# Optimization experiments

Measured on AMD Instinct MI355X. Metric: run time of the kernel, lower is better.

Reference implementation:

```python
import jax, jax.numpy as jnp
import numpy as np

N = 32768      # total nodes
E = 524288     # edges (avg degree 16)
HID = 256      # hidden_dim
H = 8          # heads
C = HID // H   # head dim = 32
G = 64         # graphs in batch
NPG = N // G   # nodes per graph = 512
EDIM = 2       # edge feature dim
NEG_SLOPE = 0.2  # PyG GATv2 default


def setup_inputs():
    key = jax.random.key(0)
    ks = jax.random.split(key, 12)
    s = 0.05
    return dict(
        x=jax.random.normal(ks[0], (N, HID), jnp.float32),
        edge_attr=jax.random.normal(ks[1], (E, EDIM), jnp.float32),
        # GATv2Conv params
        W_l=jax.random.normal(ks[2], (HID, HID), jnp.float32) * s,
        b_l=jnp.zeros((HID,), jnp.float32),
        W_r=jax.random.normal(ks[3], (HID, HID), jnp.float32) * s,
        b_r=jnp.zeros((HID,), jnp.float32),
        W_e=jax.random.normal(ks[4], (EDIM, HID), jnp.float32) * s,
        att=jax.random.normal(ks[5], (H, C), jnp.float32) * s,
        bias_gat=jnp.zeros((HID,), jnp.float32),
        # MultiheadAttention params (torch packed qkv layout)
        in_proj_w=jax.random.normal(ks[6], (3 * HID, HID), jnp.float32) * s,
        in_proj_b=jnp.zeros((3 * HID,), jnp.float32),
        out_proj_w=jax.random.normal(ks[7], (HID, HID), jnp.float32) * s,
        out_proj_b=jnp.zeros((HID,), jnp.float32),
        alpha_param=jnp.array(0.5, jnp.float32),
        # FFN
        W1=jax.random.normal(ks[8], (HID, 4 * HID), jnp.float32) * s,
        b1=jnp.zeros((4 * HID,), jnp.float32),
        W2=jax.random.normal(ks[9], (4 * HID, HID), jnp.float32) * s,
        b2=jnp.zeros((HID,), jnp.float32),
        # LayerNorms
        g1=jnp.ones((HID,), jnp.float32), be1=jnp.zeros((HID,), jnp.float32),
        g2=jnp.ones((HID,), jnp.float32), be2=jnp.zeros((HID,), jnp.float32),
        g3=jnp.ones((HID,), jnp.float32), be3=jnp.zeros((HID,), jnp.float32),
        edge_index=jax.random.randint(ks[10], (2, E), 0, N, jnp.int32),
        batch=jnp.repeat(jnp.arange(G, dtype=jnp.int32), NPG),
    )


def _ln(x, g, b, eps=1e-5):
    m = jnp.mean(x, -1, keepdims=True)
    v = jnp.mean((x - m) ** 2, -1, keepdims=True)
    return (x - m) * jax.lax.rsqrt(v + eps) * g + b


def _gatv2(x, edge_index, edge_attr, W_l, b_l, W_r, b_r, W_e, att, bias_gat):
    src, dst = edge_index[0], edge_index[1]
    # PyG add_self_loops with fill_value='mean': self-loop edge_attr at node i
    # is the mean of edge_attr over edges incoming to i (0 if none).
    deg = jax.ops.segment_sum(jnp.ones((E,), x.dtype), dst, num_segments=N)
    ea_mean = jax.ops.segment_sum(edge_attr, dst, num_segments=N) / jnp.maximum(deg, 1.0)[:, None]
    loop = jnp.arange(N, dtype=src.dtype)
    src2 = jnp.concatenate([src, loop])
    dst2 = jnp.concatenate([dst, loop])
    ea2 = jnp.concatenate([edge_attr, ea_mean], axis=0)  # [E+N, 2]
    xl = (x @ W_l + b_l).reshape(N, H, C)  # source transform (messages)
    xr = (x @ W_r + b_r).reshape(N, H, C)  # target transform
    ee = (ea2 @ W_e).reshape(-1, H, C)
    e = jax.nn.leaky_relu(xl[src2] + xr[dst2] + ee, NEG_SLOPE)  # [E+N, H, C]
    score = jnp.einsum('ehc,hc->eh', e, att)  # [E+N, H]
    # scatter softmax over incoming edges of each target node
    smax = jax.lax.stop_gradient(jax.ops.segment_max(score, dst2, num_segments=N))
    ex = jnp.exp(score - smax[dst2])
    ssum = jax.ops.segment_sum(ex, dst2, num_segments=N)
    alpha = ex / ssum[dst2]  # [E+N, H]
    out = jax.ops.segment_sum(alpha[:, :, None] * xl[src2], dst2, num_segments=N)
    return out.reshape(N, HID) + bias_gat


def _mha(xg, in_proj_w, in_proj_b, out_proj_w, out_proj_b):
    # xg: [G, NPG, HID]; torch nn.MultiheadAttention (batch_first, eval mode)
    qkv = xg @ in_proj_w.T + in_proj_b
    q, k, v = jnp.split(qkv, 3, axis=-1)
    q = q.reshape(G, NPG, H, C)
    k = k.reshape(G, NPG, H, C)
    v = v.reshape(G, NPG, H, C)
    scores = jnp.einsum('gqhd,gkhd->ghqk', q, k) / jnp.sqrt(jnp.float32(C))
    p = jax.nn.softmax(scores, axis=-1)
    o = jnp.einsum('ghqk,gkhd->gqhd', p, v).reshape(G, NPG, HID)
    return o @ out_proj_w.T + out_proj_b


def reference(x, edge_attr, W_l, b_l, W_r, b_r, W_e, att, bias_gat,
              in_proj_w, in_proj_b, out_proj_w, out_proj_b, alpha_param,
              W1, b1, W2, b2, g1, be1, g2, be2, g3, be3, edge_index, batch):
    local_out = _ln(
        _gatv2(x, edge_index, edge_attr, W_l, b_l, W_r, b_r, W_e, att, bias_gat),
        g1, be1)
    # batch is sorted with equal-sized graphs -> the per-graph ragged
    # attention loop equals one batched [G, NPG, NPG] attention
    xg = x.reshape(G, NPG, HID)
    global_out = _mha(xg, in_proj_w, in_proj_b, out_proj_w, out_proj_b).reshape(N, HID)
    global_out = _ln(global_out, g2, be2)
    a = jax.nn.sigmoid(alpha_param)
    combined = a * local_out + (1.0 - a) * global_out
    ffn = jax.nn.gelu(combined @ W1 + b1, approximate=False) @ W2 + b2
    return _ln(combined + ffn, g3, be3)
```

## Files before the change

### kernel.cpp

```cpp
#include <hip/hip_runtime.h>
#include <math.h>

#define N_NODES 32768
#define E_EDGES 524288
#define HIDDEN  256
#define NPG     512
#define NGRAPH  64
#define NHEAD   8
#define CDIM    32

typedef unsigned short bf16;
typedef __attribute__((ext_vector_type(8))) short short8;
typedef __attribute__((ext_vector_type(4))) float f4;

#define AS1 __attribute__((address_space(1)))
#define AS3 __attribute__((address_space(3)))

__device__ __forceinline__ void cp16(const bf16* g, bf16* l) {
    __builtin_amdgcn_global_load_lds((AS1 const unsigned int*)(const void*)g,
                                     (AS3 unsigned int*)(void*)l, 16, 0, 0);
}

__device__ inline float bf2f(unsigned short u) {
    union { unsigned int i; float f; } v; v.i = ((unsigned int)u) << 16; return v.f;
}
__device__ inline unsigned short f2bf(float f) {
    union { float f; unsigned int i; } v; v.f = f;
    unsigned int x = v.i;
    return (unsigned short)((x + 0x7FFFu + ((x >> 16) & 1u)) >> 16);
}
__device__ inline float4 load4(const float* p) { return *(const float4*)p; }
__device__ inline float4 load4(const bf16* p) {
    ushort4 u = *(const ushort4*)p;
    return make_float4(bf2f(u.x), bf2f(u.y), bf2f(u.z), bf2f(u.w));
}
__device__ inline void store4(float* p, float4 v) { *(float4*)p = v; }
__device__ inline void store4(bf16* p, float4 v) {
    ushort4 u; u.x = f2bf(v.x); u.y = f2bf(v.y); u.z = f2bf(v.z); u.w = f2bf(v.w);
    *(ushort4*)p = u;
}


__global__ void zero_kernel(float* deg, float* ea_sum, int* fill) {
    int i = blockIdx.x * blockDim.x + threadIdx.x;
    if (i < 2 * N_NODES) ea_sum[i] = 0.0f;
    if (i < N_NODES) { deg[i] = 0.0f; fill[i] = 0; }
}

__global__ void deg_kernel(const int* __restrict__ ei, const float* __restrict__ edge_attr,
                           float* deg, float* ea_sum) {
    int e = blockIdx.x * blockDim.x + threadIdx.x;
    if (e >= E_EDGES) return;
    int d = ei[E_EDGES + e];
    atomicAdd(&deg[d], 1.0f);
    atomicAdd(&ea_sum[2 * d + 0], edge_attr[2 * e + 0]);
    atomicAdd(&ea_sum[2 * d + 1], edge_attr[2 * e + 1]);
}

__global__ void eamean_kernel(const float* __restrict__ deg, float* ea_mean) {
    int i = blockIdx.x * blockDim.x + threadIdx.x;
    if (i >= N_NODES) return;
    float dm = fmaxf(deg[i], 1.0f);
    ea_mean[2 * i + 0] /= dm;
    ea_mean[2 * i + 1] /= dm;
}

__global__ __launch_bounds__(1024) void scan_kernel(const float* __restrict__ deg, int* row_ptr) {
    __shared__ int part[1024];
    int t = threadIdx.x;
    int base = t * 32;
    int loc[32];
    int s = 0;
    #pragma unroll
    for (int j = 0; j < 32; j++) {
        loc[j] = s;
        s += (int)deg[base + j] + 1;
    }
    int mysum = s;
    part[t] = s;
    __syncthreads();
    for (int off = 1; off < 1024; off <<= 1) {
        int v = 0;
        if (t >= off) v = part[t - off];
        __syncthreads();
        part[t] += v;
        __syncthreads();
    }
    int offset = part[t] - mysum;
    #pragma unroll
    for (int j = 0; j < 32; j++) row_ptr[base + j] = offset + loc[j];
    if (t == 1023) row_ptr[N_NODES] = part[1023];
}

__global__ void fill_kernel(const int* __restrict__ ei, const float* __restrict__ edge_attr,
                            const float* __restrict__ ea_mean,
                            const int* __restrict__ row_ptr, int* fill, int4* __restrict__ erec) {
    int tid = blockIdx.x * blockDim.x + threadIdx.x;
    if (tid >= E_EDGES + N_NODES) return;
    int d, src; float a0, a1;
    if (tid < E_EDGES) {
        d = ei[E_EDGES + tid];
        src = ei[tid];
        a0 = edge_attr[2 * tid + 0];
        a1 = edge_attr[2 * tid + 1];
    } else {
        d = tid - E_EDGES;
        src = d;
        a0 = ea_mean[2 * d + 0];
        a1 = ea_mean[2 * d + 1];
    }
    int pos = row_ptr[d] + atomicAdd(&fill[d], 1);
    int4 r;
    r.x = src;
    r.y = __float_as_int(a0);
    r.z = __float_as_int(a1);
    r.w = 0;
    erec[pos] = r;
}

__global__ void convall(const float* __restrict__ x,
                        const float* __restrict__ W_l, const float* __restrict__ W_r,
                        const float* __restrict__ W1, const float* __restrict__ W2,
                        const float* __restrict__ in_proj_w, const float* __restrict__ out_proj_w,
                        const float* __restrict__ b_l, const float* __restrict__ b_r,
                        bf16* xb, bf16* wlrb, bf16* w1b, bf16* w2b,
                        bf16* wipb, bf16* wopb, float* blr)
{
    int b = blockIdx.x, t = threadIdx.x;
    if (b < 8192) {
        int i = b * 256 + t;
        store4(&xb[i * 4], *(const float4*)&x[i * 4]);
    } else if (b < 8448) {
        int i = (b - 8192) * 256 + t; int k = i >> 8, n = i & 255;
        wlrb[n * 256 + k] = f2bf(W_l[i]);
    } else if (b < 8704) {
        int i = (b - 8448) * 256 + t; int k = i >> 8, n = i & 255;
        wlrb[(256 + n) * 256 + k] = f2bf(W_r[i]);
    } else if (b < 9728) {
        int i = (b - 8704) * 256 + t; int k = i >> 10, n = i & 1023;
        w1b[n * 256 + k] = f2bf(W1[i]);
    } else if (b < 10752) {
        int i = (b - 9728) * 256 + t; int k = i >> 8, n = i & 255;
        w2b[n * 1024 + k] = f2bf(W2[i]);
    } else if (b < 10944) {
        int i = (b - 10752) * 256 + t;
        store4(&wipb[i * 4], *(const float4*)&in_proj_w[i * 4]);
    } else if (b < 11008) {
        int i = (b - 10944) * 256 + t;
        store4(&wopb[i * 4], *(const float4*)&out_proj_w[i * 4]);
    } else {
        blr[t] = b_l[t]; blr[256 + t] = b_r[t];
    }
}

template <int EPI>
__global__ __launch_bounds__(256) void mfma_gemm(
    const bf16* __restrict__ A, const bf16* __restrict__ Wb,
    const float* __restrict__ bias, const bf16* __restrict__ res,
    bf16* __restrict__ C, int M, int N, int K)
{
    __shared__ bf16 lds[2 * 128 * 64];
    bf16* As = lds;
    bf16* Bs = lds + 128 * 64;
    int tid = threadIdx.x;
    int wave = tid >> 6, lane = tid & 63;
    int quad = lane >> 4, l16 = lane & 15;
    int n0 = blockIdx.x * 128, m0 = blockIdx.y * 128;
    int wm = (wave & 1) * 64, wn = (wave >> 1) * 64;

    f4 acc[4][4] = {};

    int srow = tid >> 3;
    int scol = (tid & 7) * 8;

    for (int k0 = 0; k0 < K; k0 += 64) {
        #pragma unroll
        for (int i = 0; i < 4; i++) {
            int row = i * 32 + srow;
            cp16(&A[(size_t)(m0 + row) * K + k0 + scol], &As[row * 64 + scol]);
            cp16(&Wb[(size_t)(n0 + row) * K + k0 + scol], &Bs[row * 64 + scol]);
        }
        __syncthreads();
        #pragma unroll
        for (int ks = 0; ks < 2; ks++) {
            short8 af[4], bfr[4];
            #pragma unroll
            for (int mt = 0; mt < 4; mt++)
                af[mt] = *(const short8*)&As[(wm + mt * 16 + l16) * 64 + ks * 32 + quad * 8];
            #pragma unroll
            for (int nt = 0; nt < 4; nt++)
                bfr[nt] = *(const short8*)&Bs[(wn + nt * 16 + l16) * 64 + ks * 32 + quad * 8];
            #pragma unroll
            for (int mt = 0; mt < 4; mt++)
                #pragma unroll
                for (int nt = 0; nt < 4; nt++)
                    acc[mt][nt] = __builtin_amdgcn_mfma_f32_16x16x32_bf16(
                        af[mt], bfr[nt], acc[mt][nt], 0, 0, 0);
        }
        __syncthreads();
    }

    float* epi = (float*)lds + wave * 16 * 68;
    int row = lane >> 2;
    int cb = (lane & 3) * 16;
    int gn = n0 + wn + cb;
    float bb[16];
    *(float4*)&bb[0]  = *(const float4*)&bias[gn + 0];
    *(float4*)&bb[4]  = *(const float4*)&bias[gn + 4];
    *(float4*)&bb[8]  = *(const float4*)&bias[gn + 8];
    *(float4*)&bb[12] = *(const float4*)&bias[gn + 12];

    for (int mt = 0; mt < 4; mt++) {
        #pragma unroll
        for (int nt = 0; nt < 4; nt++)
            #pragma unroll
            for (int r = 0; r < 4; r++)
                epi[(quad * 4 + r) * 68 + nt * 16 + l16] = acc[mt][nt][r];
        float vv[16];
        *(float4*)&vv[0]  = *(float4*)&epi[row * 68 + cb + 0];
        *(float4*)&vv[4]  = *(float4*)&epi[row * 68 + cb + 4];
        *(float4*)&vv[8]  = *(float4*)&epi[row * 68 + cb + 8];
        *(float4*)&vv[12] = *(float4*)&epi[row * 68 + cb + 12];
        int gm = m0 + wm + mt * 16 + row;
        #pragma unroll
        for (int j = 0; j < 16; j++) vv[j] += bb[j];
        if (EPI == 1) {
            #pragma unroll
            for (int j = 0; j < 16; j++)
                vv[j] = 0.5f * vv[j] * (1.0f + erff(vv[j] * 0.70710678118654752f));
        } else if (EPI == 2) {
            ushort rr[16];
            const bf16* rp = &res[(size_t)gm * N + gn];
            *(int4*)&rr[0] = *(const int4*)&rp[0];
            *(int4*)&rr[8] = *(const int4*)&rp[8];
            #pragma unroll
            for (int j = 0; j < 16; j++) vv[j] += bf2f(rr[j]);
        }
        ushort o16[16];
        #pragma unroll
        for (int j = 0; j < 16; j++) o16[j] = f2bf(vv[j]);
        bf16* cp;
        if (EPI == 3) {
            bf16* dst = (gn < 256) ? C : (bf16*)res;
            int goff = (gn < 256) ? gn : gn - 256;
            cp = &dst[(size_t)gm * 256 + goff];
        } else {
            cp = &C[(size_t)gm * N + gn];
        }
        *(int4*)&cp[0] = *(int4*)&o16[0];
        *(int4*)&cp[8] = *(int4*)&o16[8];
    }
}

__global__ __launch_bounds__(256) void attn_mfma(
    const bf16* __restrict__ qkv, bf16* __restrict__ attnout)
{
    __shared__ bf16 Ks[128 * 40];
    __shared__ bf16 Vt[32 * 136];
    __shared__ bf16 Pb[4 * 64 * 40];

    int b = blockIdx.x;
    int g = b >> 4, h = (b >> 1) & 7, hlf = b & 1;
    int tid = threadIdx.x;
    int wave = tid >> 6, lane = tid & 63;
    int quad = lane >> 4, l16 = lane & 15;
    int qbase = hlf * 256 + wave * 64;
    bf16* Pw = &Pb[wave * 64 * 40];
    const float SCALE = 0.17677669529663687f;

    short8 qf[4];
    #pragma unroll
    for (int mt = 0; mt < 4; mt++) {
        size_t node = (size_t)(g * NPG + qbase + mt * 16 + l16);
        qf[mt] = *(const short8*)&qkv[node * 768 + h * CDIM + quad * 8];
    }

    f4 oacc[4][2] = {};
    float lacc[4][4] = {};

    for (int c = 0; c < 4; c++) {
        int kk0 = c * 128;
        __syncthreads();
        #pragma unroll
        for (int i = 0; i < 2; i++) {
            int idx = i * 256 + tid;
            int key = idx >> 2, kc = (idx & 3) * 8;
            *(int4*)&Ks[key * 40 + kc] =
                *(const int4*)&qkv[(size_t)(g * NPG + kk0 + key) * 768 + 256 + h * CDIM + kc];
        }
        {
            int key = tid >> 1, dblk = (tid & 1) * 16;
            ushort tmp[16];
            const bf16* vp = &qkv[(size_t)(g * NPG + kk0 + key) * 768 + 512 + h * CDIM + dblk];
            *(int4*)&tmp[0] = *(const int4*)&vp[0];
            *(int4*)&tmp[8] = *(const int4*)&vp[8];
            #pragma unroll
            for (int j = 0; j < 16; j++) Vt[(dblk + j) * 136 + key] = tmp[j];
        }
        __syncthreads();

        for (int sub = 0; sub < 4; sub++) {
            int ks0 = sub * 32;
            short8 kf[2];
            #pragma unroll
            for (int nt = 0; nt < 2; nt++)
                kf[nt] = *(const short8*)&Ks[(ks0 + nt * 16 + l16) * 40 + quad * 8];
            #pragma unroll
            for (int mt = 0; mt < 4; mt++) {
                #pragma unroll
                for (int nt = 0; nt < 2; nt++) {
                    f4 z = {0.f, 0.f, 0.f, 0.f};
                    f4 s = __builtin_amdgcn_mfma_f32_16x16x32_bf16(qf[mt], kf[nt], z, 0, 0, 0);
                    #pragma unroll
                    for (int r = 0; r < 4; r++) {
                        float p = __expf(s[r] * SCALE);
                        lacc[mt][r] += p;
                        Pw[(mt * 16 + quad * 4 + r) * 40 + nt * 16 + l16] = f2bf(p);
                    }
                }
            }
            short8 vf[2];
            #pragma unroll
            for (int dt = 0; dt < 2; dt++)
                vf[dt] = *(const short8*)&Vt[(dt * 16 + l16) * 136 + ks0 + quad * 8];
            #pragma unroll
            for (int mt = 0; mt < 4; mt++) {
                short8 pf = *(const short8*)&Pw[(mt * 16 + l16) * 40 + quad * 8];
                #pragma unroll
                for (int dt = 0; dt < 2; dt++)
                    oacc[mt][dt] = __builtin_amdgcn_mfma_f32_16x16x32_bf16(
                        pf, vf[dt], oacc[mt][dt], 0, 0, 0);
            }
        }
    }

    #pragma unroll
    for (int mt = 0; mt < 4; mt++)
        #pragma unroll
        for (int r = 0; r < 4; r++) {
            float l = lacc[mt][r];
            l += __shfl_xor(l, 1);
            l += __shfl_xor(l, 2);
            l += __shfl_xor(l, 4);
            l += __shfl_xor(l, 8);
            lacc[mt][r] = l;
        }

    #pragma unroll
    for (int mt = 0; mt < 4; mt++) {
        #pragma unroll
        for (int dt = 0; dt < 2; dt++) {
            #pragma unroll
            for (int r = 0; r < 4; r++) {
                float v = oacc[mt][dt][r] / lacc[mt][r];
                size_t node = (size_t)(g * NPG + qbase + mt * 16 + quad * 4 + r);
                attnout[node * HIDDEN + h * CDIM + dt * 16 + l16] = f2bf(v);
            }
        }
    }
}

__device__ __forceinline__ void fetchrec(
    int i, int re, int node, const int4* __restrict__ erec,
    int& s, float& a0, float& a1)
{
    if (i < re) {
        int4 r = erec[i];
        s = r.x; a0 = __int_as_float(r.y); a1 = __int_as_float(r.z);
    } else {
        s = node; a0 = 0.f; a1 = 0.f;
    }
}

__global__ __launch_bounds__(256) void gat_kernel(
    const bf16* __restrict__ xl, const bf16* __restrict__ xr,
    const int* __restrict__ row_ptr, const int4* __restrict__ erec,
    const float* __restrict__ W_e, const float* __restrict__ att,
    const float* __restrict__ bias_gat,
    const float* __restrict__ g1, const float* __restrict__ be1,
    bf16* __restrict__ out)
{
    __shared__ float pacc[2][260];
    __shared__ float plsum[2][64];
    int wave = threadIdx.x >> 6;
    int lane = threadIdx.x & 63;
    int nloc = wave >> 1, half = wave & 1;
    int node = blockIdx.x * 2 + nloc;
    int cb = lane * 4;

    float4 xr4 = load4(&xr[(size_t)node * 256 + cb]);
    float4 we0 = *(const float4*)&W_e[cb];
    float4 we1 = *(const float4*)&W_e[HIDDEN + cb];
    float4 at4 = *(const float4*)&att[cb];

    int rs = row_ptr[node], re = row_ptr[node + 1];

    float lsum = 0.f;
    float acc0 = 0.f, acc1 = 0.f, acc2 = 0.f, acc3 = 0.f;

    int i0 = rs + half;
    int s0, s1; float a00, a01, a10, a11;
    fetchrec(i0,     re, node, erec, s0, a00, a01);
    fetchrec(i0 + 2, re, node, erec, s1, a10, a11);
    ushort4 xu0 = *(const ushort4*)&xl[(size_t)s0 * 256 + cb];

    for (int i = i0; i < re; i += 2) {
        int s2; float a20, a21;
        fetchrec(i + 4, re, node, erec, s2, a20, a21);
        ushort4 xu1 = *(const ushort4*)&xl[(size_t)s1 * 256 + cb];

        float4 xl4 = make_float4(bf2f(xu0.x), bf2f(xu0.y), bf2f(xu0.z), bf2f(xu0.w));
        float t, p = 0.f;
        t = xl4.x + xr4.x + a00 * we0.x + a01 * we1.x; t = (t > 0.f) ? t : 0.2f * t; p += t * at4.x;
        t = xl4.y + xr4.y + a00 * we0.y + a01 * we1.y; t = (t > 0.f) ? t : 0.2f * t; p += t * at4.y;
        t = xl4.z + xr4.z + a00 * we0.z + a01 * we1.z; t = (t > 0.f) ? t : 0.2f * t; p += t * at4.z;
        t = xl4.w + xr4.w + a00 * we0.w + a01 * we1.w; t = (t > 0.f) ? t : 0.2f * t; p += t * at4.w;
        p += __shfl_xor(p, 1);
        p += __shfl_xor(p, 2);
        p += __shfl_xor(p, 4);
        float w = __expf(p);
        lsum += w;
        acc0 += w * xl4.x; acc1 += w * xl4.y; acc2 += w * xl4.z; acc3 += w * xl4.w;

        s0 = s1; a00 = a10; a01 = a11; xu0 = xu1;
        s1 = s2; a10 = a20; a11 = a21;
    }

    if (half) {
        plsum[nloc][lane] = lsum;
        pacc[nloc][cb + 0] = acc0; pacc[nloc][cb + 1] = acc1;
        pacc[nloc][cb + 2] = acc2; pacc[nloc][cb + 3] = acc3;
    }
    __syncthreads();
    if (!half) {
        lsum += plsum[nloc][lane];
        acc0 += pacc[nloc][cb + 0]; acc1 += pacc[nloc][cb + 1];
        acc2 += pacc[nloc][cb + 2]; acc3 += pacc[nloc][cb + 3];

        float inv = 1.0f / lsum;
        float v0 = acc0 * inv + bias_gat[cb + 0];
        float v1 = acc1 * inv + bias_gat[cb + 1];
        float v2 = acc2 * inv + bias_gat[cb + 2];
        float v3 = acc3 * inv + bias_gat[cb + 3];

        float s = v0 + v1 + v2 + v3;
        #pragma unroll
        for (int m = 1; m < 64; m <<= 1) s += __shfl_xor(s, m);
        float mean = s * (1.0f / 256.0f);
        float d0 = v0 - mean, d1 = v1 - mean, d2 = v2 - mean, d3 = v3 - mean;
        float sq = d0 * d0 + d1 * d1 + d2 * d2 + d3 * d3;
        #pragma unroll
        for (int m = 1; m < 64; m <<= 1) sq += __shfl_xor(sq, m);
        float rstd = rsqrtf(sq * (1.0f / 256.0f) + 1e-5f);
        float4 o;
        o.x = d0 * rstd * g1[cb + 0] + be1[cb + 0];
        o.y = d1 * rstd * g1[cb + 1] + be1[cb + 1];
        o.z = d2 * rstd * g1[cb + 2] + be1[cb + 2];
        o.w = d3 * rstd * g1[cb + 3] + be1[cb + 3];
        store4(&out[(size_t)node * HIDDEN + cb], o);
    }
}

__global__ __launch_bounds__(256) void combine_kernel(
    const bf16* __restrict__ gout, const bf16* __restrict__ localout,
    const float* __restrict__ alpha_p,
    const float* __restrict__ g2, const float* __restrict__ be2,
    bf16* __restrict__ combined)
{
    int wave = threadIdx.x >> 6;
    int lane = threadIdx.x & 63;
    int node = blockIdx.x * 4 + wave;
    int cb = lane * 4;
    float4 gv = load4(&gout[(size_t)node * HIDDEN + cb]);
    float s = gv.x + gv.y + gv.z + gv.w;
    #pragma unroll
    for (int m = 1; m < 64; m <<= 1) s += __shfl_xor(s, m);
    float mean = s * (1.0f / 256.0f);
    float d0 = gv.x - mean, d1 = gv.y - mean, d2 = gv.z - mean, d3 = gv.w - mean;
    float sq = d0 * d0 + d1 * d1 + d2 * d2 + d3 * d3;
    #pragma unroll
    for (int m = 1; m < 64; m <<= 1) sq += __shfl_xor(sq, m);
    float rstd = rsqrtf(sq * (1.0f / 256.0f) + 1e-5f);
    float n0 = d0 * rstd * g2[cb + 0] + be2[cb + 0];
    float n1 = d1 * rstd * g2[cb + 1] + be2[cb + 1];
    float n2 = d2 * rstd * g2[cb + 2] + be2[cb + 2];
    float n3 = d3 * rstd * g2[cb + 3] + be2[cb + 3];
    float a = 1.0f / (1.0f + __expf(-alpha_p[0]));
    float4 lv = load4(&localout[(size_t)node * HIDDEN + cb]);
    float4 o;
    o.x = a * lv.x + (1.0f - a) * n0;
    o.y = a * lv.y + (1.0f - a) * n1;
    o.z = a * lv.z + (1.0f - a) * n2;
    o.w = a * lv.w + (1.0f - a) * n3;
    store4(&combined[(size_t)node * HIDDEN + cb], o);
}

__global__ __launch_bounds__(256) void finalln_kernel(
    const bf16* __restrict__ ffn,
    const float* __restrict__ g3, const float* __restrict__ be3,
    float* __restrict__ out)
{
    int wave = threadIdx.x >> 6;
    int lane = threadIdx.x & 63;
    int node = blockIdx.x * 4 + wave;
    int cb = lane * 4;
    float4 v = load4(&ffn[(size_t)node * HIDDEN + cb]);
    float s = v.x + v.y + v.z + v.w;
    #pragma unroll
    for (int m = 1; m < 64; m <<= 1) s += __shfl_xor(s, m);
    float mean = s * (1.0f / 256.0f);
    float d0 = v.x - mean, d1 = v.y - mean, d2 = v.z - mean, d3 = v.w - mean;
    float sq = d0 * d0 + d1 * d1 + d2 * d2 + d3 * d3;
    #pragma unroll
    for (int m = 1; m < 64; m <<= 1) sq += __shfl_xor(sq, m);
    float rstd = rsqrtf(sq * (1.0f / 256.0f) + 1e-5f);
    float4 o;
    o.x = d0 * rstd * g3[cb + 0] + be3[cb + 0];
    o.y = d1 * rstd * g3[cb + 1] + be3[cb + 1];
    o.z = d2 * rstd * g3[cb + 2] + be3[cb + 2];
    o.w = d3 * rstd * g3[cb + 3] + be3[cb + 3];
    *(float4*)&out[(size_t)node * HIDDEN + cb] = o;
}

extern "C" void kernel_launch(void* const* d_in, const int* in_sizes, int n_in,
                              void* d_out, int out_size, void* d_ws, size_t ws_size,
                              hipStream_t stream) {
    const float* x          = (const float*)d_in[0];
    const float* edge_attr  = (const float*)d_in[1];
    const float* W_l        = (const float*)d_in[2];
    const float* b_l        = (const float*)d_in[3];
    const float* W_r        = (const float*)d_in[4];
    const float* b_r        = (const float*)d_in[5];
    const float* W_e        = (const float*)d_in[6];
    const float* att        = (const float*)d_in[7];
    const float* bias_gat   = (const float*)d_in[8];
    const float* in_proj_w  = (const float*)d_in[9];
    const float* in_proj_b  = (const float*)d_in[10];
    const float* out_proj_w = (const float*)d_in[11];
    const float* out_proj_b = (const float*)d_in[12];
    const float* alpha_p    = (const float*)d_in[13];
    const float* W1         = (const float*)d_in[14];
    const float* b1         = (const float*)d_in[15];
    const float* W2         = (const float*)d_in[16];
    const float* b2         = (const float*)d_in[17];
    const float* g1  = (const float*)d_in[18];
    const float* be1 = (const float*)d_in[19];
    const float* g2  = (const float*)d_in[20];
    const float* be2 = (const float*)d_in[21];
    const float* g3  = (const float*)d_in[22];
    const float* be3 = (const float*)d_in[23];
    const int* edge_index = (const int*)d_in[24];

    char* base = (char*)d_ws;
    const size_t MB = 1024 * 1024;
    const size_t KB = 1024;
    float* deg     = (float*)(base + 0);
    float* ea_mean = (float*)(base + 131072);
    int*   fill    = (int*)  (base + 393216);
    int*   row_ptr = (int*)  (base + 524288);
    bf16* wlrb = (bf16*)(base + 3 * MB);
    bf16* wipb = (bf16*)(base + 3 * MB + 256 * KB);
    bf16* wopb = (bf16*)(base + 3 * MB + 640 * KB);
    bf16* w1b  = (bf16*)(base + 3 * MB + 768 * KB);
    bf16* w2b  = (bf16*)(base + 3 * MB + 1280 * KB);
    float* blr = (float*)(base + 5 * MB);
    bf16* xb       = (bf16*)(base + 8 * MB);
    bf16* qkv      = (bf16*)(base + 24 * MB);
    bf16* attnout  = (bf16*)(base + 72 * MB);
    bf16* gout     = (bf16*)(base + 24 * MB);
    bf16* xl       = (bf16*)(base + 40 * MB);
    bf16* xr       = (bf16*)(base + 56 * MB);
    bf16* localout = (bf16*)(base + 72 * MB);
    bf16* combined = (bf16*)(base + 8 * MB);
    bf16* h1h      = (bf16*)(base + 24 * MB);
    bf16* ffn      = (bf16*)(base + 56 * MB);
    int4* erec     = (int4*)(base + 88 * MB);
    float* out = (float*)d_out;

    zero_kernel<<<(2 * N_NODES + 255) / 256, 256, 0, stream>>>(deg, ea_mean, fill);
    deg_kernel<<<E_EDGES / 256, 256, 0, stream>>>(edge_index, edge_attr, deg, ea_mean);
    eamean_kernel<<<N_NODES / 256, 256, 0, stream>>>(deg, ea_mean);
    scan_kernel<<<1, 1024, 0, stream>>>(deg, row_ptr);
    fill_kernel<<<(E_EDGES + N_NODES + 255) / 256, 256, 0, stream>>>(
        edge_index, edge_attr, ea_mean, row_ptr, fill, erec);

    convall<<<11009, 256, 0, stream>>>(x, W_l, W_r, W1, W2, in_proj_w, out_proj_w,
                                       b_l, b_r, xb, wlrb, w1b, w2b, wipb, wopb, blr);

    mfma_gemm<0><<<dim3(6, 256), 256, 0, stream>>>(
        xb, wipb, in_proj_b, (const bf16*)nullptr, qkv, N_NODES, 768, 256);
    attn_mfma<<<NGRAPH * NHEAD * 2, 256, 0, stream>>>(qkv, attnout);
    mfma_gemm<0><<<dim3(2, 256), 256, 0, stream>>>(
        attnout, wopb, out_proj_b, (const bf16*)nullptr, gout, N_NODES, 256, 256);

    mfma_gemm<3><<<dim3(4, 256), 256, 0, stream>>>(
        xb, wlrb, blr, (const bf16*)xr, xl, N_NODES, 512, 256);
    gat_kernel<<<N_NODES / 2, 256, 0, stream>>>(
        xl, xr, row_ptr, erec, W_e, att, bias_gat, g1, be1, localout);

    combine_kernel<<<N_NODES / 4, 256, 0, stream>>>(
        gout, localout, alpha_p, g2, be2, combined);

    for (int hh = 0; hh < 2; hh++) {
        const bf16* ch = combined + (size_t)hh * 16384 * 256;
        bf16* fh = ffn + (size_t)hh * 16384 * 256;
        mfma_gemm<1><<<dim3(8, 128), 256, 0, stream>>>(
            ch, w1b, b1, (const bf16*)nullptr, h1h, 16384, 1024, 256);
        mfma_gemm<2><<<dim3(2, 128), 256, 0, stream>>>(
            h1h, w2b, b2, ch, fh, 16384, 256, 1024);
    }

    finalln_kernel<<<N_NODES / 4, 256, 0, stream>>>(ffn, g3, be3, out);
}
```

Baseline: 590.7 us.

## Fold attention scale into weights, fuse eamean, widen GAT prefetch, unsplit FFN

Result: no change. 588.5 us (-0.4%).

```diff
diff --git a/kernel.cpp b/kernel.cpp
--- a/kernel.cpp
+++ b/kernel.cpp
@@ -28,6 +28,9 @@
     union { float f; unsigned int i; } v; v.f = f;
     unsigned int x = v.i;
     return (unsigned short)((x + 0x7FFFu + ((x >> 16) & 1u)) >> 16);
+}
+__device__ inline unsigned short f2bf_trunc(float f) {
+    return (unsigned short)(__float_as_uint(f) >> 16);
 }
 __device__ inline float4 load4(const float* p) { return *(const float4*)p; }
 __device__ inline float4 load4(const bf16* p) {
@@ -55,14 +58,6 @@
     atomicAdd(&deg[d], 1.0f);
     atomicAdd(&ea_sum[2 * d + 0], edge_attr[2 * e + 0]);
     atomicAdd(&ea_sum[2 * d + 1], edge_attr[2 * e + 1]);
-}
-
-__global__ void eamean_kernel(const float* __restrict__ deg, float* ea_mean) {
-    int i = blockIdx.x * blockDim.x + threadIdx.x;
-    if (i >= N_NODES) return;
-    float dm = fmaxf(deg[i], 1.0f);
-    ea_mean[2 * i + 0] /= dm;
-    ea_mean[2 * i + 1] /= dm;
 }
 
 __global__ __launch_bounds__(1024) void scan_kernel(const float* __restrict__ deg, int* row_ptr) {
@@ -93,7 +88,7 @@
 }
 
 __global__ void fill_kernel(const int* __restrict__ ei, const float* __restrict__ edge_attr,
-                            const float* __restrict__ ea_mean,
+                            const float* __restrict__ ea_sum, const float* __restrict__ deg,
                             const int* __restrict__ row_ptr, int* fill, int4* __restrict__ erec) {
     int tid = blockIdx.x * blockDim.x + threadIdx.x;
     if (tid >= E_EDGES + N_NODES) return;
@@ -106,8 +101,9 @@
     } else {
         d = tid - E_EDGES;
         src = d;
-        a0 = ea_mean[2 * d + 0];
-        a1 = ea_mean[2 * d + 1];
+        float dm = fmaxf(deg[d], 1.0f);
+        a0 = ea_sum[2 * d + 0] / dm;
+        a1 = ea_sum[2 * d + 1] / dm;
     }
     int pos = row_ptr[d] + atomicAdd(&fill[d], 1);
     int4 r;
@@ -118,13 +114,15 @@
     erec[pos] = r;
 }
 
+#define QSCALE 0.25506882685716462f
 __global__ void convall(const float* __restrict__ x,
                         const float* __restrict__ W_l, const float* __restrict__ W_r,
                         const float* __restrict__ W1, const float* __restrict__ W2,
                         const float* __restrict__ in_proj_w, const float* __restrict__ out_proj_w,
                         const float* __restrict__ b_l, const float* __restrict__ b_r,
+                        const float* __restrict__ in_proj_b,
                         bf16* xb, bf16* wlrb, bf16* w1b, bf16* w2b,
-                        bf16* wipb, bf16* wopb, float* blr)
+                        bf16* wipb, bf16* wopb, float* blr, float* ipb2)
 {
     int b = blockIdx.x, t = threadIdx.x;
     if (b < 8192) {
@@ -144,12 +142,17 @@
         w2b[n * 1024 + k] = f2bf(W2[i]);
     } else if (b < 10944) {
         int i = (b - 10752) * 256 + t;
-        store4(&wipb[i * 4], *(const float4*)&in_proj_w[i * 4]);
+        float4 v = *(const float4*)&in_proj_w[i * 4];
+        if (i < 16384) { v.x *= QSCALE; v.y *= QSCALE; v.z *= QSCALE; v.w *= QSCALE; }
+        store4(&wipb[i * 4], v);
     } else if (b < 11008) {
         int i = (b - 10944) * 256 + t;
         store4(&wopb[i * 4], *(const float4*)&out_proj_w[i * 4]);
     } else {
         blr[t] = b_l[t]; blr[256 + t] = b_r[t];
+        ipb2[t] = in_proj_b[t] * QSCALE;
+        ipb2[256 + t] = in_proj_b[256 + t];
+        ipb2[512 + t] = in_proj_b[512 + t];
     }
 }
 
@@ -169,7 +172,6 @@
     int wm = (wave & 1) * 64, wn = (wave >> 1) * 64;
 
     f4 acc[4][4] = {};
-
     int srow = tid >> 3;
     int scol = (tid & 7) * 8;
 
@@ -228,13 +230,19 @@
             #pragma unroll
             for (int j = 0; j < 16; j++)
                 vv[j] = 0.5f * vv[j] * (1.0f + erff(vv[j] * 0.70710678118654752f));
-        } else if (EPI == 2) {
+        } else if (EPI == 4) {
             ushort rr[16];
             const bf16* rp = &res[(size_t)gm * N + gn];
             *(int4*)&rr[0] = *(const int4*)&rp[0];
             *(int4*)&rr[8] = *(const int4*)&rp[8];
             #pragma unroll
             for (int j = 0; j < 16; j++) vv[j] += bf2f(rr[j]);
+            float* cf = (float*)C + (size_t)gm * N + gn;
+            *(float4*)&cf[0]  = *(float4*)&vv[0];
+            *(float4*)&cf[4]  = *(float4*)&vv[4];
+            *(float4*)&cf[8]  = *(float4*)&vv[8];
+            *(float4*)&cf[12] = *(float4*)&vv[12];
+            continue;
         }
         ushort o16[16];
         #pragma unroll
@@ -266,7 +274,6 @@
     int quad = lane >> 4, l16 = lane & 15;
     int qbase = hlf * 256 + wave * 64;
     bf16* Pw = &Pb[wave * 64 * 40];
-    const float SCALE = 0.17677669529663687f;
 
     short8 qf[4];
     #pragma unroll
@@ -313,9 +320,9 @@
                     f4 s = __builtin_amdgcn_mfma_f32_16x16x32_bf16(qf[mt], kf[nt], z, 0, 0, 0);
                     #pragma unroll
                     for (int r = 0; r < 4; r++) {
-                        float p = __expf(s[r] * SCALE);
+                        float p = exp2f(s[r]);
                         lacc[mt][r] += p;
-                        Pw[(mt * 16 + quad * 4 + r) * 40 + nt * 16 + l16] = f2bf(p);
+                        Pw[(mt * 16 + quad * 4 + r) * 40 + nt * 16 + l16] = f2bf_trunc(p);
                     }
                 }
             }
@@ -399,15 +406,18 @@
     float acc0 = 0.f, acc1 = 0.f, acc2 = 0.f, acc3 = 0.f;
 
     int i0 = rs + half;
-    int s0, s1; float a00, a01, a10, a11;
+    int s0, s1, s2;
+    float a00, a01, a10, a11, a20, a21;
     fetchrec(i0,     re, node, erec, s0, a00, a01);
     fetchrec(i0 + 2, re, node, erec, s1, a10, a11);
+    fetchrec(i0 + 4, re, node, erec, s2, a20, a21);
     ushort4 xu0 = *(const ushort4*)&xl[(size_t)s0 * 256 + cb];
+    ushort4 xu1 = *(const ushort4*)&xl[(size_t)s1 * 256 + cb];
 
     for (int i = i0; i < re; i += 2) {
-        int s2; float a20, a21;
-        fetchrec(i + 4, re, node, erec, s2, a20, a21);
-        ushort4 xu1 = *(const ushort4*)&xl[(size_t)s1 * 256 + cb];
+        int s3; float a30, a31;
+        fetchrec(i + 6, re, node, erec, s3, a30, a31);
+        ushort4 xu2 = *(const ushort4*)&xl[(size_t)s2 * 256 + cb];
 
         float4 xl4 = make_float4(bf2f(xu0.x), bf2f(xu0.y), bf2f(xu0.z), bf2f(xu0.w));
         float t, p = 0.f;
@@ -423,7 +433,8 @@
         acc0 += w * xl4.x; acc1 += w * xl4.y; acc2 += w * xl4.z; acc3 += w * xl4.w;
 
         s0 = s1; a00 = a10; a01 = a11; xu0 = xu1;
-        s1 = s2; a10 = a20; a11 = a21;
+        s1 = s2; a10 = a20; a11 = a21; xu1 = xu2;
+        s2 = s3; a20 = a30; a21 = a31;
     }
 
     if (half) {
@@ -496,15 +507,14 @@
 }
 
 __global__ __launch_bounds__(256) void finalln_kernel(
-    const bf16* __restrict__ ffn,
-    const float* __restrict__ g3, const float* __restrict__ be3,
-    float* __restrict__ out)
+    float* __restrict__ out,
+    const float* __restrict__ g3, const float* __restrict__ be3)
 {
     int wave = threadIdx.x >> 6;
     int lane = threadIdx.x & 63;
     int node = blockIdx.x * 4 + wave;
     int cb = lane * 4;
-    float4 v = load4(&ffn[(size_t)node * HIDDEN + cb]);
+    float4 v = *(const float4*)&out[(size_t)node * HIDDEN + cb];
     float s = v.x + v.y + v.z + v.w;
     #pragma unroll
     for (int m = 1; m < 64; m <<= 1) s += __shfl_xor(s, m);
@@ -555,7 +565,7 @@
     const size_t MB = 1024 * 1024;
     const size_t KB = 1024;
     float* deg     = (float*)(base + 0);
-    float* ea_mean = (float*)(base + 131072);
+    float* ea_sum  = (float*)(base + 131072);
     int*   fill    = (int*)  (base + 393216);
     int*   row_ptr = (int*)  (base + 524288);
     bf16* wlrb = (bf16*)(base + 3 * MB);
@@ -563,7 +573,8 @@
     bf16* wopb = (bf16*)(base + 3 * MB + 640 * KB);
     bf16* w1b  = (bf16*)(base + 3 * MB + 768 * KB);
     bf16* w2b  = (bf16*)(base + 3 * MB + 1280 * KB);
-    float* blr = (float*)(base + 5 * MB);
+    float* blr  = (float*)(base + 5 * MB);
+    float* ipb2 = (float*)(base + 5 * MB + 4 * KB);
     bf16* xb       = (bf16*)(base + 8 * MB);
     bf16* qkv      = (bf16*)(base + 24 * MB);
     bf16* attnout  = (bf16*)(base + 72 * MB);
@@ -572,23 +583,22 @@
     bf16* xr       = (bf16*)(base + 56 * MB);
     bf16* localout = (bf16*)(base + 72 * MB);
     bf16* combined = (bf16*)(base + 8 * MB);
-    bf16* h1h      = (bf16*)(base + 24 * MB);
-    bf16* ffn      = (bf16*)(base + 56 * MB);
+    bf16* h1       = (bf16*)(base + 24 * MB);
     int4* erec     = (int4*)(base + 88 * MB);
     float* out = (float*)d_out;
 
-    zero_kernel<<<(2 * N_NODES + 255) / 256, 256, 0, stream>>>(deg, ea_mean, fill);
-    deg_kernel<<<E_EDGES / 256, 256, 0, stream>>>(edge_index, edge_attr, deg, ea_mean);
-    eamean_kernel<<<N_NODES / 256, 256, 0, stream>>>(deg, ea_mean);
+    zero_kernel<<<(2 * N_NODES + 255) / 256, 256, 0, stream>>>(deg, ea_sum, fill);
+    deg_kernel<<<E_EDGES / 256, 256, 0, stream>>>(edge_index, edge_attr, deg, ea_sum);
     scan_kernel<<<1, 1024, 0, stream>>>(deg, row_ptr);
     fill_kernel<<<(E_EDGES + N_NODES + 255) / 256, 256, 0, stream>>>(
-        edge_index, edge_attr, ea_mean, row_ptr, fill, erec);
+        edge_index, edge_attr, ea_sum, deg, row_ptr, fill, erec);
 
     convall<<<11009, 256, 0, stream>>>(x, W_l, W_r, W1, W2, in_proj_w, out_proj_w,
-                                       b_l, b_r, xb, wlrb, w1b, w2b, wipb, wopb, blr);
+                                       b_l, b_r, in_proj_b,
+                                       xb, wlrb, w1b, w2b, wipb, wopb, blr, ipb2);
 
     mfma_gemm<0><<<dim3(6, 256), 256, 0, stream>>>(
-        xb, wipb, in_proj_b, (const bf16*)nullptr, qkv, N_NODES, 768, 256);
+        xb, wipb, ipb2, (const bf16*)nullptr, qkv, N_NODES, 768, 256);
     attn_mfma<<<NGRAPH * NHEAD * 2, 256, 0, stream>>>(qkv, attnout);
     mfma_gemm<0><<<dim3(2, 256), 256, 0, stream>>>(
         attnout, wopb, out_proj_b, (const bf16*)nullptr, gout, N_NODES, 256, 256);
@@ -601,14 +611,10 @@
     combine_kernel<<<N_NODES / 4, 256, 0, stream>>>(
         gout, localout, alpha_p, g2, be2, combined);
 
-    for (int hh = 0; hh < 2; hh++) {
-        const bf16* ch = combined + (size_t)hh * 16384 * 256;
-        bf16* fh = ffn + (size_t)hh * 16384 * 256;
-        mfma_gemm<1><<<dim3(8, 128), 256, 0, stream>>>(
-            ch, w1b, b1, (const bf16*)nullptr, h1h, 16384, 1024, 256);
-        mfma_gemm<2><<<dim3(2, 128), 256, 0, stream>>>(
-            h1h, w2b, b2, ch, fh, 16384, 256, 1024);
-    }
-
-    finalln_kernel<<<N_NODES / 4, 256, 0, stream>>>(ffn, g3, be3, out);
-}
+    mfma_gemm<1><<<dim3(8, 256), 256, 0, stream>>>(
+        combined, w1b, b1, (const bf16*)nullptr, h1, N_NODES, 1024, 256);
+    mfma_gemm<4><<<dim3(2, 256), 256, 0, stream>>>(
+        h1, w2b, b2, combined, (bf16*)out, N_NODES, 256, 1024);
+
+    finalln_kernel<<<N_NODES / 4, 256, 0, stream>>>(out, g3, be3);
+}
```
